# Optimization experiments

Hardware: AMD Instinct MI355X
Metric: run time of the kernel (lower is better)

The kernel has to match this reference:

```python
import jax, jax.numpy as jnp
import numpy as np
from jax.ops import segment_sum


def gcn_conv(x, src, dst, W, b, num_nodes):
    # PyG GCNConv: x' = D^{-1/2} (A + I) D^{-1/2} (x @ W) + b
    loops = jnp.arange(num_nodes, dtype=src.dtype)
    s = jnp.concatenate([src, loops])  # source of each edge (incl. self-loops)
    d = jnp.concatenate([dst, loops])  # destination of each edge
    ones = jnp.ones(s.shape[0], dtype=x.dtype)
    deg = segment_sum(ones, d, num_segments=num_nodes)  # in-degree incl. self-loop
    dinv = jnp.where(deg > 0, jax.lax.rsqrt(deg), 0.0)
    norm = dinv[s] * dinv[d]  # [E+N]
    h = x @ W  # [N, C_out] dense transform first (C_out <= C_in typical)
    msg = h[s] * norm[:, None]  # gather + scale  [E+N, C_out]
    out = segment_sum(msg, d, num_segments=num_nodes)  # scatter-add
    return out + b


def setup_inputs() -> dict:
    key = jax.random.key(0)
    k1, k2, k3, k4 = jax.random.split(key, 4)
    N, E = 100000, 1600000
    C_in, C_out = 64, 32
    C_hid = 2 * C_out
    x = jax.random.normal(k1, (N, C_in), dtype=jnp.float32)
    edge_index = jax.random.randint(k2, (2, E), 0, N, dtype=jnp.int64)
    # Glorot-style init for the linear weights, zero bias (PyG defaults)
    W1 = jax.random.normal(k3, (C_in, C_hid), dtype=jnp.float32) * (1.0 / np.sqrt(C_in))
    b1 = jnp.zeros((C_hid,), dtype=jnp.float32)
    W2 = jax.random.normal(k4, (C_hid, C_out), dtype=jnp.float32) * (1.0 / np.sqrt(C_hid))
    b2 = jnp.zeros((C_out,), dtype=jnp.float32)
    return {"x": x, "edge_index": edge_index, "num_nodes": N,
            "W1": W1, "b1": b1, "W2": W2, "b2": b2}


def reference(x, edge_index, num_nodes, W1, b1, W2, b2):
    src, dst = edge_index[0], edge_index[1]
    h = gcn_conv(x, src, dst, W1, b1, num_nodes)
    h = jax.nn.relu(h)
    out = gcn_conv(h, src, dst, W2, b2, num_nodes)
    return out
```

## Files before the change

kernel.cpp:

```cpp
#include <hip/hip_runtime.h>


constexpr int CAP = 8192;
constexpr int NBMAX = 512;

__device__ inline unsigned short f2bf(float f) {
    unsigned u = __float_as_uint(f);
    u += 0x7fff + ((u >> 16) & 1);
    return (unsigned short)(u >> 16);
}
__device__ inline float bflo(unsigned u) { return __uint_as_float(u << 16); }
__device__ inline float bfhi(unsigned u) { return __uint_as_float(u & 0xffff0000u); }

__global__ __launch_bounds__(256) void p1_bin(const int* __restrict__ src,
                                              const int* __restrict__ dst,
                                              int* __restrict__ bucketCursor,
                                              unsigned* __restrict__ staging, int E, int NB) {
    __shared__ int cnt[NBMAX];
    __shared__ int cur[NBMAX];
    int tid = threadIdx.x;
    for (int i = tid; i < NB; i += 256) cnt[i] = 0;
    __syncthreads();
    int e0 = blockIdx.x * 4096;
#pragma unroll
    for (int k = 0; k < 16; ++k) {
        int e = e0 + k * 256 + tid;
        if (e < E) atomicAdd(&cnt[dst[e] >> 8], 1);
    }
    __syncthreads();
    for (int i = tid; i < NB; i += 256) {
        int c = cnt[i];
        cur[i] = c ? atomicAdd(&bucketCursor[i], c) : 0;
    }
    __syncthreads();
#pragma unroll
    for (int k = 0; k < 16; ++k) {
        int e = e0 + k * 256 + tid;
        if (e < E) {
            int d = dst[e];
            int b = d >> 8;
            int slot = atomicAdd(&cur[b], 1);
            staging[(size_t)b * CAP + slot] = ((unsigned)src[e] << 8) | (unsigned)(d & 255);
        }
    }
}

__global__ __launch_bounds__(512) void scan_buckets(const int* __restrict__ bucketCursor,
                                                    int* __restrict__ bucketBase,
                                                    int* __restrict__ rp, int NB, int N, int E) {
    __shared__ int s[NBMAX];
    int tid = threadIdx.x;
    int v = (tid < NB) ? bucketCursor[tid] : 0;
    s[tid] = v;
    __syncthreads();
    for (int off = 1; off < 512; off <<= 1) {
        int t = (tid >= off) ? s[tid - off] : 0;
        __syncthreads();
        s[tid] += t;
        __syncthreads();
    }
    if (tid < NB) bucketBase[tid] = s[tid] - v;
    if (tid == 0) {
        bucketBase[NB] = E;
        rp[N] = E;
    }
}

__global__ __launch_bounds__(256) void p2_csr(const unsigned* __restrict__ staging,
                                              const int* __restrict__ bucketBase,
                                              int* __restrict__ rp, int* __restrict__ col,
                                              float* __restrict__ dinv, int N) {
    __shared__ int deg[256];
    __shared__ int scn[256];
    __shared__ int cur[256];
    int b = blockIdx.x;
    int tid = threadIdx.x;
    int base = bucketBase[b];
    int size = bucketBase[b + 1] - base;
    const unsigned* st = staging + (size_t)b * CAP;
    deg[tid] = 0;
    __syncthreads();
    for (int i = tid; i < size; i += 256) atomicAdd(&deg[st[i] & 255u], 1);
    __syncthreads();
    int g = b * 256 + tid;
    int d = deg[tid];
    if (g < N) dinv[g] = rsqrtf((float)(d + 1));
    scn[tid] = d;
    __syncthreads();
    for (int off = 1; off < 256; off <<= 1) {
        int t = (tid >= off) ? scn[tid - off] : 0;
        __syncthreads();
        scn[tid] += t;
        __syncthreads();
    }
    int excl = scn[tid] - d;
    if (g < N) rp[g] = base + excl;
    cur[tid] = excl;
    __syncthreads();
    for (int i = tid; i < size; i += 256) {
        unsigned pk = st[i];
        int pos = atomicAdd(&cur[pk & 255u], 1);
        col[base + pos] = (int)(pk >> 8);
    }
}

template <int COUT, int TC, bool BF16OUT>
__global__ __launch_bounds__(256) void gemm_tile(const float* __restrict__ X,
                                                 const float* __restrict__ W,
                                                 const float* __restrict__ dinv,
                                                 void* __restrict__ Hout, int N) {
    constexpr int RPB = 128;
    constexpr int CG = COUT / TC;
    constexpr int XS = 65;
    __shared__ float Xs[RPB * XS];
    __shared__ float Ws[64 * COUT];
    int tid = threadIdx.x;
    int rowBase = blockIdx.x * RPB;
    const float4* Wv = (const float4*)W;
    float4* Wsv = (float4*)Ws;
    for (int i = tid; i < 64 * COUT / 4; i += 256) Wsv[i] = Wv[i];
    const float4* Xv = (const float4*)X;
    for (int v = tid; v < RPB * 16; v += 256) {
        int r = v >> 4, j = v & 15;
        int gr = rowBase + r;
        float4 t = make_float4(0.f, 0.f, 0.f, 0.f);
        if (gr < N) t = Xv[(size_t)gr * 16 + j];
        int b = r * XS + j * 4;
        Xs[b] = t.x;
        Xs[b + 1] = t.y;
        Xs[b + 2] = t.z;
        Xs[b + 3] = t.w;
    }
    __syncthreads();
    int cg = tid % CG, rg = tid / CG;
    int c0 = cg * TC, r0 = rg * 4;
    float acc[4][TC];
#pragma unroll
    for (int i = 0; i < 4; ++i)
#pragma unroll
        for (int j = 0; j < TC; ++j) acc[i][j] = 0.f;
#pragma unroll 8
    for (int k = 0; k < 64; ++k) {
        float4 w0 = *(const float4*)&Ws[k * COUT + c0];
        float4 w1;
        if (TC == 8) w1 = *(const float4*)&Ws[k * COUT + c0 + 4];
        float xr[4];
#pragma unroll
        for (int i = 0; i < 4; ++i) xr[i] = Xs[(r0 + i) * XS + k];
#pragma unroll
        for (int i = 0; i < 4; ++i) {
            acc[i][0] = fmaf(xr[i], w0.x, acc[i][0]);
            acc[i][1] = fmaf(xr[i], w0.y, acc[i][1]);
            acc[i][2] = fmaf(xr[i], w0.z, acc[i][2]);
            acc[i][3] = fmaf(xr[i], w0.w, acc[i][3]);
            if (TC == 8) {
                acc[i][4] = fmaf(xr[i], w1.x, acc[i][4]);
                acc[i][5] = fmaf(xr[i], w1.y, acc[i][5]);
                acc[i][6] = fmaf(xr[i], w1.z, acc[i][6]);
                acc[i][7] = fmaf(xr[i], w1.w, acc[i][7]);
            }
        }
    }
#pragma unroll
    for (int i = 0; i < 4; ++i) {
        int row = rowBase + r0 + i;
        if (row >= N) continue;
        float dn = dinv[row];
        if (BF16OUT) {
            unsigned pk[TC / 2];
#pragma unroll
            for (int j = 0; j < TC / 2; ++j) {
                unsigned lo = f2bf(acc[i][2 * j] * dn);
                unsigned hi = f2bf(acc[i][2 * j + 1] * dn);
                pk[j] = lo | (hi << 16);
            }
            if (TC == 8) {
                uint4 v = make_uint4(pk[0], pk[1], pk[2], pk[3]);
                *(uint4*)((unsigned short*)Hout + (size_t)row * COUT + c0) = v;
            } else {
                uint2 v = make_uint2(pk[0], pk[1]);
                *(uint2*)((unsigned short*)Hout + (size_t)row * COUT + c0) = v;
            }
        } else {
#pragma unroll
            for (int j4 = 0; j4 < TC / 4; ++j4) {
                float4 v = make_float4(acc[i][4 * j4] * dn, acc[i][4 * j4 + 1] * dn,
                                       acc[i][4 * j4 + 2] * dn, acc[i][4 * j4 + 3] * dn);
                *(float4*)((float*)Hout + (size_t)row * COUT + c0 + 4 * j4) = v;
            }
        }
    }
}

__global__ __launch_bounds__(256) void aggregate_bf16(
    const uint4* __restrict__ hs, const float* __restrict__ dinv, const int* __restrict__ rp,
    const int* __restrict__ col, const float* __restrict__ bias, float* __restrict__ out, int N) {
    int t = blockIdx.x * blockDim.x + threadIdx.x;
    int node = t >> 3, q = t & 7;
    if (node >= N) return;
    float acc[8];
    uint4 u = hs[(size_t)node * 8 + q];
    acc[0] = bflo(u.x); acc[1] = bfhi(u.x);
    acc[2] = bflo(u.y); acc[3] = bfhi(u.y);
    acc[4] = bflo(u.z); acc[5] = bfhi(u.z);
    acc[6] = bflo(u.w); acc[7] = bfhi(u.w);
    int e0 = rp[node], e1 = rp[node + 1];
    int e = e0;
#define ACC8(U)                                     \
    acc[0] += bflo(U.x); acc[1] += bfhi(U.x);       \
    acc[2] += bflo(U.y); acc[3] += bfhi(U.y);       \
    acc[4] += bflo(U.z); acc[5] += bfhi(U.z);       \
    acc[6] += bflo(U.w); acc[7] += bfhi(U.w);
    for (; e + 4 <= e1; e += 4) {
        int s0 = col[e], s1 = col[e + 1], s2 = col[e + 2], s3 = col[e + 3];
        uint4 u0 = hs[(size_t)s0 * 8 + q];
        uint4 u1 = hs[(size_t)s1 * 8 + q];
        uint4 u2 = hs[(size_t)s2 * 8 + q];
        uint4 u3 = hs[(size_t)s3 * 8 + q];
        ACC8(u0) ACC8(u1) ACC8(u2) ACC8(u3)
    }
    for (; e < e1; ++e) {
        uint4 uu = hs[(size_t)col[e] * 8 + q];
        ACC8(uu)
    }
#undef ACC8
    float dn = dinv[node];
    const float4* bv = (const float4*)bias;
    float4 b0 = bv[q * 2], b1 = bv[q * 2 + 1];
    float4 r0, r1;
    r0.x = fmaxf(fmaf(acc[0], dn, b0.x), 0.f);
    r0.y = fmaxf(fmaf(acc[1], dn, b0.y), 0.f);
    r0.z = fmaxf(fmaf(acc[2], dn, b0.z), 0.f);
    r0.w = fmaxf(fmaf(acc[3], dn, b0.w), 0.f);
    r1.x = fmaxf(fmaf(acc[4], dn, b1.x), 0.f);
    r1.y = fmaxf(fmaf(acc[5], dn, b1.y), 0.f);
    r1.z = fmaxf(fmaf(acc[6], dn, b1.z), 0.f);
    r1.w = fmaxf(fmaf(acc[7], dn, b1.w), 0.f);
    float4* ov = (float4*)(out + (size_t)node * 64 + q * 8);
    ov[0] = r0;
    ov[1] = r1;
}

template <int C, bool RELU>
__global__ void aggregate4(const float* __restrict__ hsBase, const float* __restrict__ dinv,
                           const int* __restrict__ rp, const int* __restrict__ col,
                           const float* __restrict__ bias, float* __restrict__ outBase, int N) {
    constexpr int L = C / 4;
    const float4* __restrict__ hs = (const float4*)hsBase;
    float4* __restrict__ out = (float4*)outBase;
    int t = blockIdx.x * blockDim.x + threadIdx.x;
    int node = t / L;
    int q = t % L;
    if (node >= N) return;
    float4 acc = hs[(size_t)node * L + q];
    int e0 = rp[node], e1 = rp[node + 1];
    int e = e0;
    for (; e + 4 <= e1; e += 4) {
        int s0 = col[e + 0], s1 = col[e + 1], s2 = col[e + 2], s3 = col[e + 3];
        float4 v0 = hs[(size_t)s0 * L + q];
        float4 v1 = hs[(size_t)s1 * L + q];
        float4 v2 = hs[(size_t)s2 * L + q];
        float4 v3 = hs[(size_t)s3 * L + q];
        acc.x += (v0.x + v1.x) + (v2.x + v3.x);
        acc.y += (v0.y + v1.y) + (v2.y + v3.y);
        acc.z += (v0.z + v1.z) + (v2.z + v3.z);
        acc.w += (v0.w + v1.w) + (v2.w + v3.w);
    }
    for (; e < e1; ++e) {
        float4 v = hs[(size_t)col[e] * L + q];
        acc.x += v.x;
        acc.y += v.y;
        acc.z += v.z;
        acc.w += v.w;
    }
    float dn = dinv[node];
    float4 bb = ((const float4*)bias)[q];
    float4 r;
    r.x = fmaf(acc.x, dn, bb.x);
    r.y = fmaf(acc.y, dn, bb.y);
    r.z = fmaf(acc.z, dn, bb.z);
    r.w = fmaf(acc.w, dn, bb.w);
    if (RELU) {
        r.x = fmaxf(r.x, 0.f);
        r.y = fmaxf(r.y, 0.f);
        r.z = fmaxf(r.z, 0.f);
        r.w = fmaxf(r.w, 0.f);
    }
    out[(size_t)node * L + q] = r;
}

extern "C" void kernel_launch(void* const* d_in, const int* in_sizes, int n_in,
                              void* d_out, int out_size, void* d_ws, size_t ws_size,
                              hipStream_t stream) {
    const float* x = (const float*)d_in[0];
    const int* ei = (const int*)d_in[1];
    const float* W1 = (const float*)d_in[3];
    const float* b1 = (const float*)d_in[4];
    const float* W2 = (const float*)d_in[5];
    const float* b2 = (const float*)d_in[6];

    constexpr int CIN = 64, CHID = 64, COUT = 32;
    const int N = in_sizes[0] / CIN;
    const int E = in_sizes[1] / 2;
    const int* src = ei;
    const int* dst = ei + E;
    const int NB = (N + 255) >> 8;

    char* p = (char*)d_ws;
    auto carve = [&](size_t bytes) -> void* {
        void* q = (void*)p;
        p += (bytes + 255) & ~(size_t)255;
        return q;
    };
    int* bucketCursor = (int*)carve((size_t)NB * 4);
    int* bucketBase = (int*)carve((size_t)(NB + 1) * 4);
    int* rp = (int*)carve((size_t)(N + 1) * 4);
    int* col = (int*)carve((size_t)E * 4);
    float* dinv = (float*)carve((size_t)N * 4);
    unsigned* staging = (unsigned*)carve((size_t)NB * CAP * 4);
    unsigned short* h1 = (unsigned short*)carve((size_t)N * CHID * 2);
    float* agg1 = (float*)carve((size_t)N * CHID * 4);
    float* h2 = (float*)staging;

    hipMemsetAsync(bucketCursor, 0, (size_t)NB * 4, stream);
    p1_bin<<<(E + 4095) / 4096, 256, 0, stream>>>(src, dst, bucketCursor, staging, E, NB);
    scan_buckets<<<1, 512, 0, stream>>>(bucketCursor, bucketBase, rp, NB, N, E);
    p2_csr<<<NB, 256, 0, stream>>>(staging, bucketBase, rp, col, dinv, N);

    gemm_tile<CHID, 8, true><<<(N + 127) / 128, 256, 0, stream>>>(x, W1, dinv, (void*)h1, N);
    aggregate_bf16<<<((size_t)N * 8 + 255) / 256, 256, 0, stream>>>((const uint4*)h1, dinv, rp,
                                                                    col, b1, agg1, N);
    gemm_tile<COUT, 4, false><<<(N + 127) / 128, 256, 0, stream>>>(agg1, W2, dinv, (void*)h2, N);
    aggregate4<COUT, false>
        <<<((size_t)N * (COUT / 4) + 255) / 256, 256, 0, stream>>>(h2, dinv, rp, col, b2,
                                                                   (float*)d_out, N);
}
```

Before: 229.8 us.

## Fuse layer-1 aggregation with layer-2 GEMM and store h2 in bf16

The first-layer neighbor aggregation (with bias and ReLU) is fused with the second-layer dense transform through a shared-memory tile, so the fp32 hidden activation is never written to or read back from global memory. The second-layer features are stored as bf16 and gathered with 16-byte loads, halving the bytes moved per edge in the final aggregation. This removes one kernel launch and a large intermediate buffer. In exchange, layer-2 messages lose precision from bf16 rounding.

Result: faster. 207.6 us (-9.7%).

```diff
diff --git a/kernel.cpp b/kernel.cpp
--- a/kernel.cpp
+++ b/kernel.cpp
@@ -104,23 +104,20 @@
     }
 }
 
-template <int COUT, int TC, bool BF16OUT>
-__global__ __launch_bounds__(256) void gemm_tile(const float* __restrict__ X,
-                                                 const float* __restrict__ W,
-                                                 const float* __restrict__ dinv,
-                                                 void* __restrict__ Hout, int N) {
-    constexpr int RPB = 128;
-    constexpr int CG = COUT / TC;
+__global__ __launch_bounds__(256) void gemm1(const float* __restrict__ X,
+                                             const float* __restrict__ W,
+                                             const float* __restrict__ dinv,
+                                             unsigned short* __restrict__ Hout, int N) {
     constexpr int XS = 65;
-    __shared__ float Xs[RPB * XS];
-    __shared__ float Ws[64 * COUT];
-    int tid = threadIdx.x;
-    int rowBase = blockIdx.x * RPB;
+    __shared__ float Xs[128 * XS];
+    __shared__ float Ws[64 * 64];
+    int tid = threadIdx.x;
+    int rowBase = blockIdx.x * 128;
     const float4* Wv = (const float4*)W;
     float4* Wsv = (float4*)Ws;
-    for (int i = tid; i < 64 * COUT / 4; i += 256) Wsv[i] = Wv[i];
+    for (int i = tid; i < 64 * 64 / 4; i += 256) Wsv[i] = Wv[i];
     const float4* Xv = (const float4*)X;
-    for (int v = tid; v < RPB * 16; v += 256) {
+    for (int v = tid; v < 128 * 16; v += 256) {
         int r = v >> 4, j = v & 15;
         int gr = rowBase + r;
         float4 t = make_float4(0.f, 0.f, 0.f, 0.f);
@@ -132,18 +129,17 @@
         Xs[b + 3] = t.w;
     }
     __syncthreads();
-    int cg = tid % CG, rg = tid / CG;
-    int c0 = cg * TC, r0 = rg * 4;
-    float acc[4][TC];
+    int cg = tid % 8, rg = tid / 8;
+    int c0 = cg * 8, r0 = rg * 4;
+    float acc[4][8];
 #pragma unroll
     for (int i = 0; i < 4; ++i)
 #pragma unroll
-        for (int j = 0; j < TC; ++j) acc[i][j] = 0.f;
+        for (int j = 0; j < 8; ++j) acc[i][j] = 0.f;
 #pragma unroll 8
     for (int k = 0; k < 64; ++k) {
-        float4 w0 = *(const float4*)&Ws[k * COUT + c0];
-        float4 w1;
-        if (TC == 8) w1 = *(const float4*)&Ws[k * COUT + c0 + 4];
+        float4 w0 = *(const float4*)&Ws[k * 64 + c0];
+        float4 w1 = *(const float4*)&Ws[k * 64 + c0 + 4];
         float xr[4];
 #pragma unroll
         for (int i = 0; i < 4; ++i) xr[i] = Xs[(r0 + i) * XS + k];
@@ -153,12 +149,10 @@
             acc[i][1] = fmaf(xr[i], w0.y, acc[i][1]);
             acc[i][2] = fmaf(xr[i], w0.z, acc[i][2]);
             acc[i][3] = fmaf(xr[i], w0.w, acc[i][3]);
-            if (TC == 8) {
-                acc[i][4] = fmaf(xr[i], w1.x, acc[i][4]);
-                acc[i][5] = fmaf(xr[i], w1.y, acc[i][5]);
-                acc[i][6] = fmaf(xr[i], w1.z, acc[i][6]);
-                acc[i][7] = fmaf(xr[i], w1.w, acc[i][7]);
-            }
+            acc[i][4] = fmaf(xr[i], w1.x, acc[i][4]);
+            acc[i][5] = fmaf(xr[i], w1.y, acc[i][5]);
+            acc[i][6] = fmaf(xr[i], w1.z, acc[i][6]);
+            acc[i][7] = fmaf(xr[i], w1.w, acc[i][7]);
         }
     }
 #pragma unroll
@@ -166,61 +160,143 @@
         int row = rowBase + r0 + i;
         if (row >= N) continue;
         float dn = dinv[row];
-        if (BF16OUT) {
-            unsigned pk[TC / 2];
-#pragma unroll
-            for (int j = 0; j < TC / 2; ++j) {
-                unsigned lo = f2bf(acc[i][2 * j] * dn);
-                unsigned hi = f2bf(acc[i][2 * j + 1] * dn);
-                pk[j] = lo | (hi << 16);
-            }
-            if (TC == 8) {
-                uint4 v = make_uint4(pk[0], pk[1], pk[2], pk[3]);
-                *(uint4*)((unsigned short*)Hout + (size_t)row * COUT + c0) = v;
-            } else {
-                uint2 v = make_uint2(pk[0], pk[1]);
-                *(uint2*)((unsigned short*)Hout + (size_t)row * COUT + c0) = v;
-            }
-        } else {
-#pragma unroll
-            for (int j4 = 0; j4 < TC / 4; ++j4) {
-                float4 v = make_float4(acc[i][4 * j4] * dn, acc[i][4 * j4 + 1] * dn,
-                                       acc[i][4 * j4 + 2] * dn, acc[i][4 * j4 + 3] * dn);
-                *(float4*)((float*)Hout + (size_t)row * COUT + c0 + 4 * j4) = v;
-            }
-        }
-    }
-}
-
-__global__ __launch_bounds__(256) void aggregate_bf16(
-    const uint4* __restrict__ hs, const float* __restrict__ dinv, const int* __restrict__ rp,
-    const int* __restrict__ col, const float* __restrict__ bias, float* __restrict__ out, int N) {
+        unsigned pk[4];
+#pragma unroll
+        for (int j = 0; j < 4; ++j) {
+            unsigned lo = f2bf(acc[i][2 * j] * dn);
+            unsigned hi = f2bf(acc[i][2 * j + 1] * dn);
+            pk[j] = lo | (hi << 16);
+        }
+        *(uint4*)(Hout + (size_t)row * 64 + c0) = make_uint4(pk[0], pk[1], pk[2], pk[3]);
+    }
+}
+
+__global__ __launch_bounds__(256) void agg1_gemm2(
+    const uint4* __restrict__ hs1, const float* __restrict__ dinv, const int* __restrict__ rp,
+    const int* __restrict__ col, const float* __restrict__ b1, const float* __restrict__ W2,
+    unsigned short* __restrict__ h2, int N) {
+    constexpr int RS = 68;
+    __shared__ float rows[32 * RS];
+    __shared__ float Ws2[64 * 32];
+    int tid = threadIdx.x;
+    const float4* W2v = (const float4*)W2;
+    float4* Ws2v = (float4*)Ws2;
+    for (int i = tid; i < 64 * 32 / 4; i += 256) Ws2v[i] = W2v[i];
+
+    int r = tid >> 3, q = tid & 7;
+    int node = blockIdx.x * 32 + r;
+    float acc[8];
+#pragma unroll
+    for (int j = 0; j < 8; ++j) acc[j] = 0.f;
+    float dn = 0.f;
+    if (node < N) {
+        dn = dinv[node];
+        uint4 u = hs1[(size_t)node * 8 + q];
+        acc[0] = bflo(u.x); acc[1] = bfhi(u.x);
+        acc[2] = bflo(u.y); acc[3] = bfhi(u.y);
+        acc[4] = bflo(u.z); acc[5] = bfhi(u.z);
+        acc[6] = bflo(u.w); acc[7] = bfhi(u.w);
+        int e0 = rp[node], e1 = rp[node + 1];
+        int e = e0;
+#define ACC8(U)                               \
+    acc[0] += bflo(U.x); acc[1] += bfhi(U.x); \
+    acc[2] += bflo(U.y); acc[3] += bfhi(U.y); \
+    acc[4] += bflo(U.z); acc[5] += bfhi(U.z); \
+    acc[6] += bflo(U.w); acc[7] += bfhi(U.w);
+        for (; e + 4 <= e1; e += 4) {
+            int s0 = col[e], s1 = col[e + 1], s2 = col[e + 2], s3 = col[e + 3];
+            uint4 u0 = hs1[(size_t)s0 * 8 + q];
+            uint4 u1 = hs1[(size_t)s1 * 8 + q];
+            uint4 u2 = hs1[(size_t)s2 * 8 + q];
+            uint4 u3 = hs1[(size_t)s3 * 8 + q];
+            ACC8(u0) ACC8(u1) ACC8(u2) ACC8(u3)
+        }
+        for (; e < e1; ++e) {
+            uint4 uu = hs1[(size_t)col[e] * 8 + q];
+            ACC8(uu)
+        }
+#undef ACC8
+        const float4* bv = (const float4*)b1;
+        float4 bb0 = bv[q * 2], bb1 = bv[q * 2 + 1];
+        acc[0] = fmaxf(fmaf(acc[0], dn, bb0.x), 0.f);
+        acc[1] = fmaxf(fmaf(acc[1], dn, bb0.y), 0.f);
+        acc[2] = fmaxf(fmaf(acc[2], dn, bb0.z), 0.f);
+        acc[3] = fmaxf(fmaf(acc[3], dn, bb0.w), 0.f);
+        acc[4] = fmaxf(fmaf(acc[4], dn, bb1.x), 0.f);
+        acc[5] = fmaxf(fmaf(acc[5], dn, bb1.y), 0.f);
+        acc[6] = fmaxf(fmaf(acc[6], dn, bb1.z), 0.f);
+        acc[7] = fmaxf(fmaf(acc[7], dn, bb1.w), 0.f);
+    }
+    float* myrow = &rows[r * RS + q * 8];
+    *(float4*)myrow = make_float4(acc[0], acc[1], acc[2], acc[3]);
+    *(float4*)(myrow + 4) = make_float4(acc[4], acc[5], acc[6], acc[7]);
+    __syncthreads();
+
+    if (node >= N) return;
+    int c0 = q * 4;
+    float acc2[4] = {0.f, 0.f, 0.f, 0.f};
+    const float* row = &rows[r * RS];
+#pragma unroll
+    for (int k4 = 0; k4 < 16; ++k4) {
+        float4 xq = *(const float4*)&row[k4 * 4];
+        float4 wa = *(const float4*)&Ws2[(k4 * 4 + 0) * 32 + c0];
+        float4 wb = *(const float4*)&Ws2[(k4 * 4 + 1) * 32 + c0];
+        float4 wc = *(const float4*)&Ws2[(k4 * 4 + 2) * 32 + c0];
+        float4 wd = *(const float4*)&Ws2[(k4 * 4 + 3) * 32 + c0];
+        acc2[0] = fmaf(xq.x, wa.x, acc2[0]);
+        acc2[1] = fmaf(xq.x, wa.y, acc2[1]);
+        acc2[2] = fmaf(xq.x, wa.z, acc2[2]);
+        acc2[3] = fmaf(xq.x, wa.w, acc2[3]);
+        acc2[0] = fmaf(xq.y, wb.x, acc2[0]);
+        acc2[1] = fmaf(xq.y, wb.y, acc2[1]);
+        acc2[2] = fmaf(xq.y, wb.z, acc2[2]);
+        acc2[3] = fmaf(xq.y, wb.w, acc2[3]);
+        acc2[0] = fmaf(xq.z, wc.x, acc2[0]);
+        acc2[1] = fmaf(xq.z, wc.y, acc2[1]);
+        acc2[2] = fmaf(xq.z, wc.z, acc2[2]);
+        acc2[3] = fmaf(xq.z, wc.w, acc2[3]);
+        acc2[0] = fmaf(xq.w, wd.x, acc2[0]);
+        acc2[1] = fmaf(xq.w, wd.y, acc2[1]);
+        acc2[2] = fmaf(xq.w, wd.z, acc2[2]);
+        acc2[3] = fmaf(xq.w, wd.w, acc2[3]);
+    }
+    unsigned p0 = f2bf(acc2[0] * dn) | ((unsigned)f2bf(acc2[1] * dn) << 16);
+    unsigned p1 = f2bf(acc2[2] * dn) | ((unsigned)f2bf(acc2[3] * dn) << 16);
+    *(uint2*)(h2 + (size_t)node * 32 + c0) = make_uint2(p0, p1);
+}
+
+__global__ __launch_bounds__(256) void agg2(const uint4* __restrict__ hs2,
+                                            const float* __restrict__ dinv,
+                                            const int* __restrict__ rp,
+                                            const int* __restrict__ col,
+                                            const float* __restrict__ bias,
+                                            float* __restrict__ out, int N) {
     int t = blockIdx.x * blockDim.x + threadIdx.x;
-    int node = t >> 3, q = t & 7;
+    int node = t >> 2, q = t & 3;
     if (node >= N) return;
     float acc[8];
-    uint4 u = hs[(size_t)node * 8 + q];
+    uint4 u = hs2[(size_t)node * 4 + q];
     acc[0] = bflo(u.x); acc[1] = bfhi(u.x);
     acc[2] = bflo(u.y); acc[3] = bfhi(u.y);
     acc[4] = bflo(u.z); acc[5] = bfhi(u.z);
     acc[6] = bflo(u.w); acc[7] = bfhi(u.w);
     int e0 = rp[node], e1 = rp[node + 1];
     int e = e0;
-#define ACC8(U)                                     \
-    acc[0] += bflo(U.x); acc[1] += bfhi(U.x);       \
-    acc[2] += bflo(U.y); acc[3] += bfhi(U.y);       \
-    acc[4] += bflo(U.z); acc[5] += bfhi(U.z);       \
+#define ACC8(U)                               \
+    acc[0] += bflo(U.x); acc[1] += bfhi(U.x); \
+    acc[2] += bflo(U.y); acc[3] += bfhi(U.y); \
+    acc[4] += bflo(U.z); acc[5] += bfhi(U.z); \
     acc[6] += bflo(U.w); acc[7] += bfhi(U.w);
     for (; e + 4 <= e1; e += 4) {
         int s0 = col[e], s1 = col[e + 1], s2 = col[e + 2], s3 = col[e + 3];
-        uint4 u0 = hs[(size_t)s0 * 8 + q];
-        uint4 u1 = hs[(size_t)s1 * 8 + q];
-        uint4 u2 = hs[(size_t)s2 * 8 + q];
-        uint4 u3 = hs[(size_t)s3 * 8 + q];
+        uint4 u0 = hs2[(size_t)s0 * 4 + q];
+        uint4 u1 = hs2[(size_t)s1 * 4 + q];
+        uint4 u2 = hs2[(size_t)s2 * 4 + q];
+        uint4 u3 = hs2[(size_t)s3 * 4 + q];
         ACC8(u0) ACC8(u1) ACC8(u2) ACC8(u3)
     }
     for (; e < e1; ++e) {
-        uint4 uu = hs[(size_t)col[e] * 8 + q];
+        uint4 uu = hs2[(size_t)col[e] * 4 + q];
         ACC8(uu)
     }
 #undef ACC8
@@ -228,65 +304,17 @@
     const float4* bv = (const float4*)bias;
     float4 b0 = bv[q * 2], b1 = bv[q * 2 + 1];
     float4 r0, r1;
-    r0.x = fmaxf(fmaf(acc[0], dn, b0.x), 0.f);
-    r0.y = fmaxf(fmaf(acc[1], dn, b0.y), 0.f);
-    r0.z = fmaxf(fmaf(acc[2], dn, b0.z), 0.f);
-    r0.w = fmaxf(fmaf(acc[3], dn, b0.w), 0.f);
-    r1.x = fmaxf(fmaf(acc[4], dn, b1.x), 0.f);
-    r1.y = fmaxf(fmaf(acc[5], dn, b1.y), 0.f);
-    r1.z = fmaxf(fmaf(acc[6], dn, b1.z), 0.f);
-    r1.w = fmaxf(fmaf(acc[7], dn, b1.w), 0.f);
-    float4* ov = (float4*)(out + (size_t)node * 64 + q * 8);
+    r0.x = fmaf(acc[0], dn, b0.x);
+    r0.y = fmaf(acc[1], dn, b0.y);
+    r0.z = fmaf(acc[2], dn, b0.z);
+    r0.w = fmaf(acc[3], dn, b0.w);
+    r1.x = fmaf(acc[4], dn, b1.x);
+    r1.y = fmaf(acc[5], dn, b1.y);
+    r1.z = fmaf(acc[6], dn, b1.z);
+    r1.w = fmaf(acc[7], dn, b1.w);
+    float4* ov = (float4*)(out + (size_t)node * 32 + q * 8);
     ov[0] = r0;
     ov[1] = r1;
-}
-
-template <int C, bool RELU>
-__global__ void aggregate4(const float* __restrict__ hsBase, const float* __restrict__ dinv,
-                           const int* __restrict__ rp, const int* __restrict__ col,
-                           const float* __restrict__ bias, float* __restrict__ outBase, int N) {
-    constexpr int L = C / 4;
-    const float4* __restrict__ hs = (const float4*)hsBase;
-    float4* __restrict__ out = (float4*)outBase;
-    int t = blockIdx.x * blockDim.x + threadIdx.x;
-    int node = t / L;
-    int q = t % L;
-    if (node >= N) return;
-    float4 acc = hs[(size_t)node * L + q];
-    int e0 = rp[node], e1 = rp[node + 1];
-    int e = e0;
-    for (; e + 4 <= e1; e += 4) {
-        int s0 = col[e + 0], s1 = col[e + 1], s2 = col[e + 2], s3 = col[e + 3];
-        float4 v0 = hs[(size_t)s0 * L + q];
-        float4 v1 = hs[(size_t)s1 * L + q];
-        float4 v2 = hs[(size_t)s2 * L + q];
-        float4 v3 = hs[(size_t)s3 * L + q];
-        acc.x += (v0.x + v1.x) + (v2.x + v3.x);
-        acc.y += (v0.y + v1.y) + (v2.y + v3.y);
-        acc.z += (v0.z + v1.z) + (v2.z + v3.z);
-        acc.w += (v0.w + v1.w) + (v2.w + v3.w);
-    }
-    for (; e < e1; ++e) {
-        float4 v = hs[(size_t)col[e] * L + q];
-        acc.x += v.x;
-        acc.y += v.y;
-        acc.z += v.z;
-        acc.w += v.w;
-    }
-    float dn = dinv[node];
-    float4 bb = ((const float4*)bias)[q];
-    float4 r;
-    r.x = fmaf(acc.x, dn, bb.x);
-    r.y = fmaf(acc.y, dn, bb.y);
-    r.z = fmaf(acc.z, dn, bb.z);
-    r.w = fmaf(acc.w, dn, bb.w);
-    if (RELU) {
-        r.x = fmaxf(r.x, 0.f);
-        r.y = fmaxf(r.y, 0.f);
-        r.z = fmaxf(r.z, 0.f);
-        r.w = fmaxf(r.w, 0.f);
-    }
-    out[(size_t)node * L + q] = r;
 }
 
 extern "C" void kernel_launch(void* const* d_in, const int* in_sizes, int n_in,
@@ -299,7 +327,7 @@
     const float* W2 = (const float*)d_in[5];
     const float* b2 = (const float*)d_in[6];
 
-    constexpr int CIN = 64, CHID = 64, COUT = 32;
+    constexpr int CIN = 64, CHID = 64;
     const int N = in_sizes[0] / CIN;
     const int E = in_sizes[1] / 2;
     const int* src = ei;
@@ -319,19 +347,15 @@
     float* dinv = (float*)carve((size_t)N * 4);
     unsigned* staging = (unsigned*)carve((size_t)NB * CAP * 4);
     unsigned short* h1 = (unsigned short*)carve((size_t)N * CHID * 2);
-    float* agg1 = (float*)carve((size_t)N * CHID * 4);
-    float* h2 = (float*)staging;
+    unsigned short* h2 = (unsigned short*)staging;
 
     hipMemsetAsync(bucketCursor, 0, (size_t)NB * 4, stream);
     p1_bin<<<(E + 4095) / 4096, 256, 0, stream>>>(src, dst, bucketCursor, staging, E, NB);
     scan_buckets<<<1, 512, 0, stream>>>(bucketCursor, bucketBase, rp, NB, N, E);
     p2_csr<<<NB, 256, 0, stream>>>(staging, bucketBase, rp, col, dinv, N);
 
-    gemm_tile<CHID, 8, true><<<(N + 127) / 128, 256, 0, stream>>>(x, W1, dinv, (void*)h1, N);
-    aggregate_bf16<<<((size_t)N * 8 + 255) / 256, 256, 0, stream>>>((const uint4*)h1, dinv, rp,
-                                                                    col, b1, agg1, N);
-    gemm_tile<COUT, 4, false><<<(N + 127) / 128, 256, 0, stream>>>(agg1, W2, dinv, (void*)h2, N);
-    aggregate4<COUT, false>
-        <<<((size_t)N * (COUT / 4) + 255) / 256, 256, 0, stream>>>(h2, dinv, rp, col, b2,
-                                                                   (float*)d_out, N);
-}
+    gemm1<<<(N + 127) / 128, 256, 0, stream>>>(x, W1, dinv, h1, N);
+    agg1_gemm2<<<(N + 31) / 32, 256, 0, stream>>>((const uint4*)h1, dinv, rp, col, b1, W2, h2, N);
+    agg2<<<((size_t)N * 4 + 255) / 256, 256, 0, stream>>>((const uint4*)h2, dinv, rp, col, b2,
+                                                          (float*)d_out, N);
+}
```
